# Optimization experiments

Hardware: AMD Instinct MI355X
Metric: run time of the kernel (lower is better)

The kernel has to match this reference:

```python
import jax, jax.numpy as jnp
import numpy as np
import math

D_MODEL = 1024
N_HEADS = 16
HEAD_DIM = D_MODEL // N_HEADS
B, S = 2, 2048


def setup_inputs() -> dict:
    key = jax.random.key(0)
    ks = jax.random.split(key, 12)
    sd = 1.0 / math.sqrt(D_MODEL)
    inp = {
        "x": jax.random.normal(ks[0], (B, S, D_MODEL), dtype=jnp.float32),
        "time_gaps": jax.random.uniform(ks[1], (B, S, 1), dtype=jnp.float32),
        "mask": jnp.ones((B, S), dtype=jnp.int32),
        "Wq": jax.random.normal(ks[2], (D_MODEL, D_MODEL), dtype=jnp.float32) * sd,
        "bq": jnp.zeros((D_MODEL,), dtype=jnp.float32),
        "Wk": jax.random.normal(ks[3], (D_MODEL, D_MODEL), dtype=jnp.float32) * sd,
        "bk": jnp.zeros((D_MODEL,), dtype=jnp.float32),
        "Wv": jax.random.normal(ks[4], (D_MODEL, D_MODEL), dtype=jnp.float32) * sd,
        "bv": jnp.zeros((D_MODEL,), dtype=jnp.float32),
        "Wo": jax.random.normal(ks[5], (D_MODEL, D_MODEL), dtype=jnp.float32) * sd,
        "bo": jnp.zeros((D_MODEL,), dtype=jnp.float32),
        "Wt": jax.random.normal(ks[6], (D_MODEL, 1), dtype=jnp.float32),
        "bt": jnp.zeros((D_MODEL,), dtype=jnp.float32),
    }
    return inp


def reference(x, time_gaps, mask, Wq, bq, Wk, bk, Wv, bv, Wo, bo, Wt, bt):
    Bb, Ss, _ = x.shape
    # time embedding: Linear(1, d_model)
    time_emb = time_gaps @ Wt.T + bt            # [B,S,D]
    x_time = x + time_emb

    def split_heads(t):
        return t.reshape(Bb, Ss, N_HEADS, HEAD_DIM).transpose(0, 2, 1, 3)  # [B,H,S,d]

    q = split_heads(x_time @ Wq.T + bq)
    k = split_heads(x_time @ Wk.T + bk)
    v = split_heads(x @ Wv.T + bv)

    scores = jnp.einsum('bhqd,bhkd->bhqk', q, k) / math.sqrt(HEAD_DIM)
    # padding mask: mask==0 positions set to -1e9 (mask broadcast as [B,1,1,S])
    pad = (mask == 0)[:, None, None, :]
    scores = jnp.where(pad, -1e9, scores)
    # causal mask
    causal = jnp.triu(jnp.ones((Ss, Ss), dtype=bool), k=1)
    scores = jnp.where(causal, -1e9, scores)

    attn = jax.nn.softmax(scores, axis=-1)      # dropout is identity in eval
    out = jnp.einsum('bhqk,bhkd->bhqd', attn, v)
    out = out.transpose(0, 2, 1, 3).reshape(Bb, Ss, D_MODEL)
    return out @ Wo.T + bo
```

## Files before the change

### kernel.cpp

```cpp
#include <hip/hip_runtime.h>

typedef short v8s __attribute__((ext_vector_type(8)));
typedef short v4s __attribute__((ext_vector_type(4)));
typedef float v4f __attribute__((ext_vector_type(4)));
typedef int   v4i __attribute__((ext_vector_type(4)));

constexpr int Bb = 2, S = 2048, D = 1024, H = 16;
constexpr int M = Bb * S;

#define DEV __device__ __forceinline__

DEV short f2bf(float f){
  unsigned u = __builtin_bit_cast(unsigned, f);
  u = (u + 0x7FFF + ((u >> 16) & 1)) >> 16;
  return (short)u;
}

DEV int swz(int r){ return (r ^ (r >> 2)) & 7; }

DEV int cvtpk(float lo, float hi){
  int r;
  asm("v_cvt_pk_bf16_f32 %0, %1, %2" : "=v"(r) : "v"(lo), "v"(hi));
  return r;
}

DEV float max3f(float a, float b, float c){
  float r;
  asm("v_max3_f32 %0, %1, %2, %3" : "=v"(r) : "v"(a), "v"(b), "v"(c));
  return r;
}

#define EXP2 exp2f

#define GLDS(gp, lp) __builtin_amdgcn_global_load_lds( \
    (const __attribute__((address_space(1))) void*)(gp), \
    (__attribute__((address_space(3))) void*)(lp), 16, 0, 0)

struct PrepArgs {
  const float* x; const float* tg; const float* Wt; const float* bt;
  const float* Ws0; const float* Ws1; const float* Ws2; const float* Ws3;
  short* Wd0; short* Wd1; short* Wd2; short* Wd3;
  short* xb; short* xtb;
};
__global__ void prep_all(PrepArgs a){
  const int bx = blockIdx.x;
  if (bx < 4096){
    int i = bx * 256 + threadIdx.x;
    int row = i >> 8;
    int c4  = i & 255;
    float4 xv = reinterpret_cast<const float4*>(a.x)[i];
    float4 wv = reinterpret_cast<const float4*>(a.Wt)[c4];
    float4 bv = reinterpret_cast<const float4*>(a.bt)[c4];
    float g = a.tg[row];
    float xs[4] = {xv.x, xv.y, xv.z, xv.w};
    float ws[4] = {wv.x, wv.y, wv.z, wv.w};
    float bs[4] = {bv.x, bv.y, bv.z, bv.w};
    v4s p, q;
    #pragma unroll
    for (int e = 0; e < 4; ++e){
      p[e] = f2bf(xs[e]);
      q[e] = f2bf(xs[e] + g * ws[e] + bs[e]);
    }
    *reinterpret_cast<v4s*>(&a.xb[(size_t)i * 4])  = p;
    *reinterpret_cast<v4s*>(&a.xtb[(size_t)i * 4]) = q;
  } else {
    const int bi = bx - 4096;
    const int widx = bi >> 10;
    const float* src = widx == 0 ? a.Ws0 : widx == 1 ? a.Ws1 : widx == 2 ? a.Ws2 : a.Ws3;
    short* dst = widx == 0 ? a.Wd0 : widx == 1 ? a.Wd1 : widx == 2 ? a.Wd2 : a.Wd3;
    int i = (bi & 1023) * 256 + threadIdx.x;
    float4 v = reinterpret_cast<const float4*>(src)[i];
    v4s o; o[0] = f2bf(v.x); o[1] = f2bf(v.y); o[2] = f2bf(v.z); o[3] = f2bf(v.w);
    *reinterpret_cast<v4s*>(&dst[(size_t)i * 4]) = o;
  }
}

template<int MODE>
DEV void gemm_core(short* lds,
                   const short* __restrict__ A, const short* __restrict__ Bw,
                   const float* __restrict__ bias, float alpha, void* __restrict__ Cout,
                   int ldc, int m0, int n0){
  short* As = lds;
  short* Bs = lds + 2 * 128 * 64;
  const int t = threadIdx.x;
  const int w = t >> 6, l = t & 63;
  const int wm = (w >> 1) * 64, wn = (w & 1) * 64;

  v4f acc[4][4] = {};

  auto stage = [&](int kt, int buf){
    const int k0 = kt * 64;
    #pragma unroll
    for (int j = 0; j < 4; ++j){
      const int cix = j * 256 + t;
      const int row = cix >> 3;
      const int c   = (cix & 7) ^ swz(row);
      GLDS(A  + (size_t)(m0 + row) * D + k0 + c * 8, As + buf * 8192 + cix * 8);
      GLDS(Bw + (size_t)(n0 + row) * D + k0 + c * 8, Bs + buf * 8192 + cix * 8);
    }
  };

  stage(0, 0);
  for (int kt = 0; kt < 16; ++kt){
    const int cur = kt & 1;
    __syncthreads();
    if (kt < 15) stage(kt + 1, cur ^ 1);
    #pragma unroll
    for (int kk = 0; kk < 2; ++kk){
      v8s af[4], bfr[4];
      #pragma unroll
      for (int mi = 0; mi < 4; ++mi){
        const int R = wm + mi * 16 + (l & 15);
        af[mi] = *reinterpret_cast<const v8s*>(&As[cur * 8192 + R * 64 + (((kk * 4 + (l >> 4)) ^ swz(R)) * 8)]);
      }
      #pragma unroll
      for (int ni = 0; ni < 4; ++ni){
        const int R = wn + ni * 16 + (l & 15);
        bfr[ni] = *reinterpret_cast<const v8s*>(&Bs[cur * 8192 + R * 64 + (((kk * 4 + (l >> 4)) ^ swz(R)) * 8)]);
      }
      __builtin_amdgcn_s_setprio(1);
      #pragma unroll
      for (int mi = 0; mi < 4; ++mi)
        #pragma unroll
        for (int ni = 0; ni < 4; ++ni)
          acc[mi][ni] = __builtin_amdgcn_mfma_f32_16x16x32_bf16(af[mi], bfr[ni], acc[mi][ni], 0, 0, 0);
      __builtin_amdgcn_s_setprio(0);
    }
  }

  #pragma unroll
  for (int mi = 0; mi < 4; ++mi){
    const int row = m0 + wm + mi * 16 + (l >> 4) * 4;
    #pragma unroll
    for (int ni = 0; ni < 4; ++ni){
      const int col = n0 + wn + ni * 16 + (l & 15);
      const float bcol = (MODE == 1) ? 0.f : bias[col];
      #pragma unroll
      for (int r = 0; r < 4; ++r){
        float bsel = (MODE == 1) ? bias[row + r] : bcol;
        float val = (acc[mi][ni][r] + bsel) * alpha;
        reinterpret_cast<short*>(Cout)[(size_t)(row + r) * ldc + col] = f2bf(val);
      }
    }
  }
}

__global__ __launch_bounds__(256, 2)
void gemm_qkv(const short* __restrict__ xtb, const short* __restrict__ xb,
              const short* __restrict__ Wqb, const short* __restrict__ Wkb,
              const short* __restrict__ Wvb,
              const float* __restrict__ bq, const float* __restrict__ bk,
              const float* __restrict__ bv, float qalpha,
              short* __restrict__ Qb, short* __restrict__ Kb, short* __restrict__ VTb){
  __shared__ short lds[4 * 128 * 64];
  const int id = blockIdx.x;
  if (id < 512){
    const int li = id;
    const int yq = li >> 5;
    const bool isK = yq >= 8;
    gemm_core<0>(lds, xtb, isK ? Wkb : Wqb, isK ? bk : bq, isK ? 1.0f : qalpha,
                 isK ? (void*)Kb : (void*)Qb, D, (li & 31) * 128, (yq & 7) * 128);
  } else {
    const int li = id - 512;
    gemm_core<1>(lds, Wvb, xb, bv, 1.0f, VTb, M, (li & 7) * 128, (li >> 3) * 128);
  }
}

__global__ __launch_bounds__(256, 3)
void gemm_o(const short* __restrict__ A, const short* __restrict__ Bw,
            const float* __restrict__ bias, float* __restrict__ C){
  __shared__ short As[2][64 * 64];
  __shared__ short Bs[2][128 * 64];
  const int t = threadIdx.x;
  const int w = t >> 6, l = t & 63;
  const int m0 = blockIdx.x * 64, n0 = blockIdx.y * 128;
  const int wm = (w >> 1) * 32, wn = (w & 1) * 64;

  v4f acc[2][4] = {};

  auto stage = [&](int kt, int buf){
    const int k0 = kt * 64;
    #pragma unroll
    for (int j = 0; j < 2; ++j){
      const int cix = j * 256 + t;
      const int row = cix >> 3;
      const int c   = (cix & 7) ^ swz(row);
      GLDS(A + (size_t)(m0 + row) * D + k0 + c * 8, &As[buf][cix * 8]);
    }
    #pragma unroll
    for (int j = 0; j < 4; ++j){
      const int cix = j * 256 + t;
      const int row = cix >> 3;
      const int c   = (cix & 7) ^ swz(row);
      GLDS(Bw + (size_t)(n0 + row) * D + k0 + c * 8, &Bs[buf][cix * 8]);
    }
  };

  stage(0, 0);
  for (int kt = 0; kt < 16; ++kt){
    const int cur = kt & 1;
    __syncthreads();
    if (kt < 15) stage(kt + 1, cur ^ 1);
    #pragma unroll
    for (int kk = 0; kk < 2; ++kk){
      v8s af[2], bfr[4];
      #pragma unroll
      for (int mi = 0; mi < 2; ++mi){
        const int R = wm + mi * 16 + (l & 15);
        af[mi] = *reinterpret_cast<const v8s*>(&As[cur][R * 64 + (((kk * 4 + (l >> 4)) ^ swz(R)) * 8)]);
      }
      #pragma unroll
      for (int ni = 0; ni < 4; ++ni){
        const int R = wn + ni * 16 + (l & 15);
        bfr[ni] = *reinterpret_cast<const v8s*>(&Bs[cur][R * 64 + (((kk * 4 + (l >> 4)) ^ swz(R)) * 8)]);
      }
      __builtin_amdgcn_s_setprio(1);
      #pragma unroll
      for (int mi = 0; mi < 2; ++mi)
        #pragma unroll
        for (int ni = 0; ni < 4; ++ni)
          acc[mi][ni] = __builtin_amdgcn_mfma_f32_16x16x32_bf16(af[mi], bfr[ni], acc[mi][ni], 0, 0, 0);
      __builtin_amdgcn_s_setprio(0);
    }
  }

  #pragma unroll
  for (int mi = 0; mi < 2; ++mi){
    const int row = m0 + wm + mi * 16 + (l >> 4) * 4;
    #pragma unroll
    for (int ni = 0; ni < 4; ++ni){
      const int col = n0 + wn + ni * 16 + (l & 15);
      const float bcol = bias[col];
      #pragma unroll
      for (int r = 0; r < 4; ++r)
        C[(size_t)(row + r) * D + col] = acc[mi][ni][r] + bcol;
    }
  }
}

__global__ __launch_bounds__(256, 4)
void attn_kernel(const short* __restrict__ Q, const short* __restrict__ K,
                 const short* __restrict__ VT, const int* __restrict__ maskp,
                 short* __restrict__ O){
  __shared__ short Ks[2][64 * 64];
  __shared__ short Vs[2][64 * 64];
  __shared__ int mflag;
  const int t = threadIdx.x, w = t >> 6, l = t & 63;
  const int g = l >> 4, q16 = l & 15;
  const int bh = blockIdx.x, b = bh >> 4, h = bh & 15;
  const int yy = (int)blockIdx.y;
  const int qx = (yy < 8) ? 31 - yy : (yy < 16) ? yy - 8 : (yy < 24) ? 39 - yy : yy - 16;
  const int q0 = qx * 64;
  const int qw = q0 + w * 16;
  const int qg = qw + q16;
  const int nkt = qx + 1;

  if (t == 0) mflag = 1;
  __syncthreads();
  {
    bool ok = true;
    const int tot = nkt * 64;
    for (int i = t * 4; i < tot; i += 1024){
      v4i mm = *reinterpret_cast<const v4i*>(&maskp[b * S + i]);
      ok = ok && (mm[0] != 0) && (mm[1] != 0) && (mm[2] != 0) && (mm[3] != 0);
    }
    if (!__all(ok)) mflag = 0;
  }
  __syncthreads();
  const bool ALLV = (mflag != 0);

  v8s qf[2];
  #pragma unroll
  for (int kc = 0; kc < 2; ++kc)
    qf[kc] = *reinterpret_cast<const v8s*>(
        &Q[(size_t)(b * S + qg) * D + h * 64 + kc * 32 + g * 8]);

  int kOff[4][2], vOff[4][2];
  #pragma unroll
  for (int nt = 0; nt < 4; ++nt){
    const int R = 32 * (nt >> 1) + 8 * (q16 >> 2) + 4 * (nt & 1) + (l & 3);
    #pragma unroll
    for (int kc = 0; kc < 2; ++kc)
      kOff[nt][kc] = R * 64 + (((kc * 4 + g) ^ swz(R)) * 8);
  }
  #pragma unroll
  for (int dt = 0; dt < 4; ++dt){
    const int R = dt * 16 + q16;
    #pragma unroll
    for (int kc = 0; kc < 2; ++kc)
      vOff[dt][kc] = R * 64 + (((kc * 4 + g) ^ swz(R)) * 8);
  }

  v4f accOT[4] = {};
  v4f accL = {};
  float mrow = -1e30f;

  const v4i onesW = {0x3F803F80, 0x3F803F80, 0x3F803F80, 0x3F803F80};
  const v8s onesv = __builtin_bit_cast(v8s, onesW);

  auto stage = [&](int kt){
    const int buf = kt & 1;
    const int kv0 = kt * 64;
    #pragma unroll
    for (int j = 0; j < 2; ++j){
      const int cix = j * 256 + t;
      const int row = cix >> 3;
      const int c   = (cix & 7) ^ swz(row);
      GLDS(K  + (size_t)(b * S + kv0 + row) * D + h * 64 + c * 8, &Ks[buf][cix * 8]);
      GLDS(VT + (size_t)(h * 64 + row) * M + b * S + kv0 + c * 8, &Vs[buf][cix * 8]);
    }
  };

  auto softmax_pv = [&](float (&p)[16], const short* vb){
    float t0 = max3f(p[0], p[1], p[2]);
    float t1 = max3f(p[3], p[4], p[5]);
    float t2 = max3f(p[6], p[7], p[8]);
    float t3 = max3f(p[9], p[10], p[11]);
    float t4 = max3f(p[12], p[13], p[14]);
    float tm = max3f(max3f(t0, t1, t2), t3, fmaxf(t4, p[15]));
    if (!__all(tm <= mrow + 8.0f)){
      float tmax = fmaxf(tm, __shfl_xor(tm, 16));
      tmax = fmaxf(tmax, __shfl_xor(tmax, 32));
      const float mnew = fmaxf(mrow, tmax);
      const float resc = EXP2(mrow - mnew);
      #pragma unroll
      for (int dt = 0; dt < 4; ++dt) accOT[dt] *= resc;
      accL *= resc;
      mrow = mnew;
    }
    #pragma unroll
    for (int j = 0; j < 16; ++j) p[j] = EXP2(p[j] - mrow);

    int pb[2][4];
    #pragma unroll
    for (int kc = 0; kc < 2; ++kc)
      #pragma unroll
      for (int s = 0; s < 4; ++s){
        const int base = (2 * kc + (s >> 1)) * 4 + (s & 1) * 2;
        pb[kc][s] = cvtpk(p[base], p[base + 1]);
      }

    __builtin_amdgcn_s_setprio(1);
    #pragma unroll
    for (int kc = 0; kc < 2; ++kc){
      v4i tmp = {pb[kc][0], pb[kc][1], pb[kc][2], pb[kc][3]};
      v8s pbv = __builtin_bit_cast(v8s, tmp);
      accL = __builtin_amdgcn_mfma_f32_16x16x32_bf16(onesv, pbv, accL, 0, 0, 0);
      #pragma unroll
      for (int dt = 0; dt < 4; ++dt){
        v8s vf = *reinterpret_cast<const v8s*>(vb + vOff[dt][kc]);
        accOT[dt] = __builtin_amdgcn_mfma_f32_16x16x32_bf16(vf, pbv, accOT[dt], 0, 0, 0);
      }
    }
    __builtin_amdgcn_s_setprio(0);
  };

  auto qk = [&](const short* kb, v4f (&sc)[4]){
    __builtin_amdgcn_s_setprio(1);
    #pragma unroll
    for (int nt = 0; nt < 4; ++nt)
      #pragma unroll
      for (int kc = 0; kc < 2; ++kc){
        v8s kf = *reinterpret_cast<const v8s*>(kb + kOff[nt][kc]);
        sc[nt] = __builtin_amdgcn_mfma_f32_16x16x32_bf16(kf, qf[kc], sc[nt], 0, 0, 0);
      }
    __builtin_amdgcn_s_setprio(0);
  };

  stage(0);

  if (ALLV){
    for (int kt = 0; kt < nkt; ++kt){
      asm volatile("s_waitcnt vmcnt(0)" ::: "memory");
      __builtin_amdgcn_s_barrier();
      if (kt + 1 < nkt) stage(kt + 1);

      const short* kb = Ks[kt & 1];
      const short* vb = Vs[kt & 1];

      v4f sc[4] = {};
      qk(kb, sc);

      float p[16];
      if (kt < qx){
        #pragma unroll
        for (int j = 0; j < 16; ++j) p[j] = sc[j >> 2][j & 3];
      } else {
        const int kv0 = kt * 64;
        #pragma unroll
        for (int nt = 0; nt < 4; ++nt)
          #pragma unroll
          for (int r = 0; r < 4; ++r){
            const int kvg = kv0 + 32 * (nt >> 1) + 8 * g + 4 * (nt & 1) + r;
            p[nt * 4 + r] = (kvg > qg) ? -1e30f : sc[nt][r];
          }
      }
      softmax_pv(p, vb);
    }
  } else {
    for (int kt = 0; kt < nkt; ++kt){
      asm volatile("s_waitcnt vmcnt(0)" ::: "memory");
      __builtin_amdgcn_s_barrier();
      if (kt + 1 < nkt) stage(kt + 1);

      const short* kb = Ks[kt & 1];
      const short* vb = Vs[kt & 1];
      const int kv0 = kt * 64;

      v4i mq[4];
      #pragma unroll
      for (int nt = 0; nt < 4; ++nt)
        mq[nt] = *reinterpret_cast<const v4i*>(
            &maskp[b * S + kv0 + 32 * (nt >> 1) + 8 * g + 4 * (nt & 1)]);

      v4f sc[4] = {};
      qk(kb, sc);

      float p[16];
      #pragma unroll
      for (int nt = 0; nt < 4; ++nt)
        #pragma unroll
        for (int r = 0; r < 4; ++r){
          const int kvg = kv0 + 32 * (nt >> 1) + 8 * g + 4 * (nt & 1) + r;
          const int kvx = (mq[nt][r] != 0) ? kvg : 0x7fffffff;
          p[nt * 4 + r] = (kvx > qg) ? -1e30f : sc[nt][r];
        }
      softmax_pv(p, vb);
    }
  }

  const float inv = 1.0f / accL[0];
  #pragma unroll
  for (int dt = 0; dt < 4; ++dt){
    v4s o4;
    #pragma unroll
    for (int r = 0; r < 4; ++r) o4[r] = f2bf(accOT[dt][r] * inv);
    *reinterpret_cast<v4s*>(
        &O[(size_t)(b * S + qg) * D + h * 64 + dt * 16 + g * 4]) = o4;
  }
}

extern "C" void kernel_launch(void* const* d_in, const int* in_sizes, int n_in,
                              void* d_out, int out_size, void* d_ws, size_t ws_size,
                              hipStream_t stream){
  const float* x   = (const float*)d_in[0];
  const float* tg  = (const float*)d_in[1];
  const int*   msk = (const int*)d_in[2];
  const float* Wq  = (const float*)d_in[3];
  const float* bq  = (const float*)d_in[4];
  const float* Wk  = (const float*)d_in[5];
  const float* bk  = (const float*)d_in[6];
  const float* Wv  = (const float*)d_in[7];
  const float* bv  = (const float*)d_in[8];
  const float* Wo  = (const float*)d_in[9];
  const float* bo  = (const float*)d_in[10];
  const float* Wt  = (const float*)d_in[11];
  const float* bt  = (const float*)d_in[12];

  char* ws = (char*)d_ws;
  const size_t MB = 1u << 20;
  short* xb  = (short*)(ws);
  short* xtb = (short*)(ws + 8 * MB);
  short* Wqb = (short*)(ws + 16 * MB);
  short* Wkb = (short*)(ws + 18 * MB);
  short* Wvb = (short*)(ws + 20 * MB);
  short* Wob = (short*)(ws + 22 * MB);
  short* Qb  = (short*)(ws + 24 * MB);
  short* Kb  = (short*)(ws + 32 * MB);
  short* VTb = (short*)(ws + 40 * MB);
  short* Ab  = (short*)(ws + 48 * MB);

  PrepArgs pa;
  pa.x = x; pa.tg = tg; pa.Wt = Wt; pa.bt = bt;
  pa.Ws0 = Wq; pa.Ws1 = Wk; pa.Ws2 = Wv; pa.Ws3 = Wo;
  pa.Wd0 = Wqb; pa.Wd1 = Wkb; pa.Wd2 = Wvb; pa.Wd3 = Wob;
  pa.xb = xb; pa.xtb = xtb;
  prep_all<<<8192, 256, 0, stream>>>(pa);

  const float qalpha = 0.125f * 1.4426950408889634f;
  gemm_qkv<<<768, 256, 0, stream>>>(xtb, xb, Wqb, Wkb, Wvb, bq, bk, bv, qalpha,
                                    Qb, Kb, VTb);

  attn_kernel<<<dim3(Bb * H, 32), 256, 0, stream>>>(Qb, Kb, VTb, msk, Ab);

  gemm_o<<<dim3(M / 64, D / 128), 256, 0, stream>>>(Ab, Wob, bo, (float*)d_out);
}
```

Baseline: 105.2 us.

## Split long causal query tiles across two KV halves and add combine kernel

Query tiles in the upper half of the sequence are each split into two blocks, and each block processes half of the causal KV range. Each block writes an unnormalized bf16 partial output plus its row max and row sum to workspace. A new combine kernel merges the two halves with log-sum-exp rescaling. The goal is to shorten the critical path set by the longest causal rows and balance work across CUs, at the cost of an extra launch, extra memory traffic, and bf16 rounding of the partial outputs.

```diff
diff --git a/kernel.cpp b/kernel.cpp
--- a/kernel.cpp
+++ b/kernel.cpp
@@ -7,6 +7,7 @@
 
 constexpr int Bb = 2, S = 2048, D = 1024, H = 16;
 constexpr int M = Bb * S;
+constexpr int PART_BYTES = 8704;
 
 #define DEV __device__ __forceinline__
 
@@ -14,6 +15,10 @@
   unsigned u = __builtin_bit_cast(unsigned, f);
   u = (u + 0x7FFF + ((u >> 16) & 1)) >> 16;
   return (short)u;
+}
+
+DEV float bf2f(short s){
+  return __builtin_bit_cast(float, ((unsigned)(unsigned short)s) << 16);
 }
 
 DEV int swz(int r){ return (r ^ (r >> 2)) & 7; }
@@ -241,7 +246,7 @@
 __global__ __launch_bounds__(256, 4)
 void attn_kernel(const short* __restrict__ Q, const short* __restrict__ K,
                  const short* __restrict__ VT, const int* __restrict__ maskp,
-                 short* __restrict__ O){
+                 short* __restrict__ O, char* __restrict__ parts){
   __shared__ short Ks[2][64 * 64];
   __shared__ short Vs[2][64 * 64];
   __shared__ int mflag;
@@ -249,18 +254,28 @@
   const int g = l >> 4, q16 = l & 15;
   const int bh = blockIdx.x, b = bh >> 4, h = bh & 15;
   const int yy = (int)blockIdx.y;
-  const int qx = (yy < 8) ? 31 - yy : (yy < 16) ? yy - 8 : (yy < 24) ? 39 - yy : yy - 16;
-  const int q0 = qx * 64;
-  const int qw = q0 + w * 16;
-  const int qg = qw + q16;
-  const int nkt = qx + 1;
+
+  int qx, klo, khi, half;
+  bool partial;
+  if (yy < 16){
+    qx = yy; klo = 0; khi = qx; half = 0; partial = false;
+  } else {
+    const int s = yy - 16;
+    qx = 16 + (s >> 1);
+    half = s & 1;
+    const int mid = (qx + 1) >> 1;
+    klo = half ? mid : 0;
+    khi = half ? qx : mid - 1;
+    partial = true;
+  }
+  const int qg = qx * 64 + w * 16 + q16;
 
   if (t == 0) mflag = 1;
   __syncthreads();
   {
     bool ok = true;
-    const int tot = nkt * 64;
-    for (int i = t * 4; i < tot; i += 1024){
+    const int lo64 = klo * 64, hi64 = (khi + 1) * 64;
+    for (int i = lo64 + t * 4; i < hi64; i += 1024){
       v4i mm = *reinterpret_cast<const v4i*>(&maskp[b * S + i]);
       ok = ok && (mm[0] != 0) && (mm[1] != 0) && (mm[2] != 0) && (mm[3] != 0);
     }
@@ -299,7 +314,7 @@
   const v8s onesv = __builtin_bit_cast(v8s, onesW);
 
   auto stage = [&](int kt){
-    const int buf = kt & 1;
+    const int buf = (kt - klo) & 1;
     const int kv0 = kt * 64;
     #pragma unroll
     for (int j = 0; j < 2; ++j){
@@ -367,16 +382,17 @@
     __builtin_amdgcn_s_setprio(0);
   };
 
-  stage(0);
+  stage(klo);
 
   if (ALLV){
-    for (int kt = 0; kt < nkt; ++kt){
+    for (int kt = klo; kt <= khi; ++kt){
       asm volatile("s_waitcnt vmcnt(0)" ::: "memory");
       __builtin_amdgcn_s_barrier();
-      if (kt + 1 < nkt) stage(kt + 1);
-
-      const short* kb = Ks[kt & 1];
-      const short* vb = Vs[kt & 1];
+      if (kt + 1 <= khi) stage(kt + 1);
+
+      const int ii = (kt - klo) & 1;
+      const short* kb = Ks[ii];
+      const short* vb = Vs[ii];
 
       v4f sc[4] = {};
       qk(kb, sc);
@@ -398,13 +414,14 @@
       softmax_pv(p, vb);
     }
   } else {
-    for (int kt = 0; kt < nkt; ++kt){
+    for (int kt = klo; kt <= khi; ++kt){
       asm volatile("s_waitcnt vmcnt(0)" ::: "memory");
       __builtin_amdgcn_s_barrier();
-      if (kt + 1 < nkt) stage(kt + 1);
-
-      const short* kb = Ks[kt & 1];
-      const short* vb = Vs[kt & 1];
+      if (kt + 1 <= khi) stage(kt + 1);
+
+      const int ii = (kt - klo) & 1;
+      const short* kb = Ks[ii];
+      const short* vb = Vs[ii];
       const int kv0 = kt * 64;
 
       v4i mq[4];
@@ -429,14 +446,66 @@
     }
   }
 
-  const float inv = 1.0f / accL[0];
+  if (!partial){
+    const float inv = 1.0f / accL[0];
+    #pragma unroll
+    for (int dt = 0; dt < 4; ++dt){
+      v4s o4;
+      #pragma unroll
+      for (int r = 0; r < 4; ++r) o4[r] = f2bf(accOT[dt][r] * inv);
+      *reinterpret_cast<v4s*>(
+          &O[(size_t)(b * S + qg) * D + h * 64 + dt * 16 + g * 4]) = o4;
+    }
+  } else {
+    char* pp = parts + (size_t)((bh * 16 + (qx - 16)) * 2 + half) * PART_BYTES;
+    short* Op = (short*)pp;
+    float* lp = (float*)(pp + 8192);
+    float* mp = (float*)(pp + 8448);
+    const int qloc = w * 16 + q16;
+    #pragma unroll
+    for (int dt = 0; dt < 4; ++dt){
+      v4s o4;
+      #pragma unroll
+      for (int r = 0; r < 4; ++r) o4[r] = f2bf(accOT[dt][r]);
+      *reinterpret_cast<v4s*>(&Op[qloc * 64 + dt * 16 + g * 4]) = o4;
+    }
+    if (g == 0){ lp[qloc] = accL[0]; mp[qloc] = mrow; }
+  }
+}
+
+__global__ __launch_bounds__(256)
+void combine_kernel(const char* __restrict__ parts, short* __restrict__ O){
+  const int bh = blockIdx.x, b = bh >> 4, h = bh & 15;
+  const int qxs = 16 + (int)blockIdx.y;
+  const int t = threadIdx.x;
+  const int q = t >> 2, dg = (t & 3) * 16;
+
+  const char* p0 = parts + (size_t)((bh * 16 + (qxs - 16)) * 2 + 0) * PART_BYTES;
+  const char* p1 = p0 + PART_BYTES;
+  const short* O0 = (const short*)p0;
+  const short* O1 = (const short*)p1;
+  const float* l0 = (const float*)(p0 + 8192);
+  const float* l1 = (const float*)(p1 + 8192);
+  const float* m0 = (const float*)(p0 + 8448);
+  const float* m1 = (const float*)(p1 + 8448);
+
+  const float mm0 = m0[q], mm1 = m1[q];
+  const float m  = fmaxf(mm0, mm1);
+  const float a0 = exp2f(mm0 - m);
+  const float a1 = exp2f(mm1 - m);
+  const float inv = 1.0f / (a0 * l0[q] + a1 * l1[q]);
+  const float c0 = a0 * inv, c1 = a1 * inv;
+
   #pragma unroll
-  for (int dt = 0; dt < 4; ++dt){
-    v4s o4;
-    #pragma unroll
-    for (int r = 0; r < 4; ++r) o4[r] = f2bf(accOT[dt][r] * inv);
-    *reinterpret_cast<v4s*>(
-        &O[(size_t)(b * S + qg) * D + h * 64 + dt * 16 + g * 4]) = o4;
+  for (int j = 0; j < 2; ++j){
+    v8s u0 = *reinterpret_cast<const v8s*>(&O0[q * 64 + dg + j * 8]);
+    v8s u1 = *reinterpret_cast<const v8s*>(&O1[q * 64 + dg + j * 8]);
+    v8s out;
+    #pragma unroll
+    for (int e = 0; e < 8; ++e)
+      out[e] = f2bf(c0 * bf2f(u0[e]) + c1 * bf2f(u1[e]));
+    *reinterpret_cast<v8s*>(
+        &O[(size_t)(b * S + qxs * 64 + q) * D + h * 64 + dg + j * 8]) = out;
   }
 }
 
@@ -469,6 +538,7 @@
   short* Kb  = (short*)(ws + 32 * MB);
   short* VTb = (short*)(ws + 40 * MB);
   short* Ab  = (short*)(ws + 48 * MB);
+  char* parts = ws;
 
   PrepArgs pa;
   pa.x = x; pa.tg = tg; pa.Wt = Wt; pa.bt = bt;
@@ -481,7 +551,8 @@
   gemm_qkv<<<768, 256, 0, stream>>>(xtb, xb, Wqb, Wkb, Wvb, bq, bk, bv, qalpha,
                                     Qb, Kb, VTb);
 
-  attn_kernel<<<dim3(Bb * H, 32), 256, 0, stream>>>(Qb, Kb, VTb, msk, Ab);
+  attn_kernel<<<dim3(Bb * H, 48), 256, 0, stream>>>(Qb, Kb, VTb, msk, Ab, parts);
+  combine_kernel<<<dim3(Bb * H, 16), 256, 0, stream>>>(parts, Ab);
 
   gemm_o<<<dim3(M / 64, D / 128), 256, 0, stream>>>(Ab, Wob, bo, (float*)d_out);
 }
```

Result: slower. 110.3 us (+4.8%).
